# Performance work log

Measured on AMD Instinct MI355X. Metric: run time of the kernel, lower is better.

Reference implementation:

```python
import jax, jax.numpy as jnp
import numpy as np

N1 = 8000   # solute nodes
N2 = 8000   # solvent nodes
E = 128000  # edges per graph side (avg degree 16)
B = 128     # number of graphs in the batch
NFEAT, NHID, NCLS = 128, 256, 512
D = 2 * NCLS   # Set2Set input dim (1024)
H = D          # LSTM hidden = input_dim in DGL Set2Set


def setup_inputs() -> dict:
    key = jax.random.key(0)
    ks = jax.random.split(key, 24)
    w = lambda k, shp, fan: (jax.random.normal(k, shp, jnp.float32) / np.sqrt(fan))
    inp = {}
    inp["x1"] = jax.random.normal(ks[0], (N1, NFEAT), jnp.float32)
    inp["x2"] = jax.random.normal(ks[1], (N2, NFEAT), jnp.float32)
    inp["src1"] = jax.random.randint(ks[2], (E,), 0, N1, jnp.int32)
    inp["dst1"] = jax.random.randint(ks[3], (E,), 0, N1, jnp.int32)
    inp["src2"] = jax.random.randint(ks[4], (E,), 0, N2, jnp.int32)
    inp["dst2"] = jax.random.randint(ks[5], (E,), 0, N2, jnp.int32)
    inp["gid1"] = jnp.sort(jax.random.randint(ks[6], (N1,), 0, B, jnp.int32))
    inp["gid2"] = jnp.sort(jax.random.randint(ks[7], (N2,), 0, B, jnp.int32))
    # GraphConv weights (DGL stores W as [in, out]) + biases
    inp["W_gc1"] = w(ks[8], (NFEAT, NHID), NFEAT); inp["b_gc1"] = jnp.zeros((NHID,), jnp.float32)
    inp["W_gc2"] = w(ks[9], (NHID, NCLS), NHID);   inp["b_gc2"] = jnp.zeros((NCLS,), jnp.float32)
    inp["W_gc3"] = w(ks[10], (NFEAT, NHID), NFEAT); inp["b_gc3"] = jnp.zeros((NHID,), jnp.float32)
    inp["W_gc4"] = w(ks[11], (NHID, NCLS), NHID);   inp["b_gc4"] = jnp.zeros((NCLS,), jnp.float32)
    # Set2Set LSTM (input = 2*D, hidden = H), torch gate order i,f,g,o
    inp["W_ih"] = w(ks[12], (4 * H, 2 * D), 2 * D)
    inp["W_hh"] = w(ks[13], (4 * H, H), H)
    inp["b_ih"] = jnp.zeros((4 * H,), jnp.float32)
    inp["b_hh"] = jnp.zeros((4 * H,), jnp.float32)
    # MLP head
    inp["W_fc1"] = w(ks[14], (1024, 4096), 4096); inp["b_fc1"] = jnp.zeros((1024,), jnp.float32)
    inp["W_fc2"] = w(ks[15], (512, 1024), 1024);  inp["b_fc2"] = jnp.zeros((512,), jnp.float32)
    inp["W_fc3"] = w(ks[16], (1, 512), 512);      inp["b_fc3"] = jnp.zeros((1,), jnp.float32)
    return inp


def _gconv(x, src, dst, W, b, n):
    # DGL GraphConv, norm='both': D_out^{-1/2} scaling at src, sum over in-edges, D_in^{-1/2} at dst
    ones = jnp.ones(src.shape[0], x.dtype)
    outd = jnp.clip(jax.ops.segment_sum(ones, src, num_segments=n), 1.0)
    ind = jnp.clip(jax.ops.segment_sum(ones, dst, num_segments=n), 1.0)
    h = (x * (outd ** -0.5)[:, None]) @ W
    agg = jax.ops.segment_sum(h[src], dst, num_segments=n)   # sparse neighbor aggregation
    return agg * (ind ** -0.5)[:, None] + b


def _set2set(x, gid, Wih, Whh, bih, bhh):
    # DGL Set2Set, n_iters=2, 1-layer LSTM; x: [N, D], gid: [N] graph membership
    d = x.shape[1]
    q_star = jnp.zeros((B, 2 * d), x.dtype)
    h = jnp.zeros((B, d), x.dtype)
    c = jnp.zeros((B, d), x.dtype)
    for _ in range(2):
        gates = q_star @ Wih.T + h @ Whh.T + bih + bhh
        i, f, g, o = jnp.split(gates, 4, axis=1)
        c = jax.nn.sigmoid(f) * c + jax.nn.sigmoid(i) * jnp.tanh(g)
        h = jax.nn.sigmoid(o) * jnp.tanh(c)
        e = jnp.sum(x * h[gid], axis=1)                       # per-node attention logit
        m = jax.ops.segment_max(e, gid, num_segments=B)
        ex = jnp.exp(e - m[gid])
        s = jax.ops.segment_sum(ex, gid, num_segments=B)
        alpha = ex / s[gid]                                   # segment softmax
        r = jax.ops.segment_sum(alpha[:, None] * x, gid, num_segments=B)
        q_star = jnp.concatenate([h, r], axis=1)
    return q_star


def reference(x1, x2, src1, dst1, src2, dst2, gid1, gid2,
              W_gc1, b_gc1, W_gc2, b_gc2, W_gc3, b_gc3, W_gc4, b_gc4,
              W_ih, W_hh, b_ih, b_hh,
              W_fc1, b_fc1, W_fc2, b_fc2, W_fc3, b_fc3):
    s = jax.nn.relu(_gconv(x1, src1, dst1, W_gc1, b_gc1, N1))
    s = _gconv(s, src1, dst1, W_gc2, b_gc2, N1)
    v = jax.nn.relu(_gconv(x2, src2, dst2, W_gc3, b_gc3, N2))
    v = _gconv(v, src2, dst2, W_gc4, b_gc4, N2)
    # len_map = len1.T @ len2 == same-graph indicator for binary membership matrices
    len_map = (gid1[:, None] == gid2[None, :]).astype(s.dtype)
    imap = jnp.tanh(s @ v.T) * len_map                        # [N1, N2]
    solvent_prime = imap.T @ s                                # [N2, NCLS]
    solute_prime = imap @ v                                   # [N1, NCLS]
    sf = jnp.concatenate([s, solute_prime], axis=1)           # [N1, 2*NCLS]
    vf = jnp.concatenate([v, solvent_prime], axis=1)
    ss = _set2set(sf, gid1, W_ih, W_hh, b_ih, b_hh)           # [B, 4*NCLS]
    vs = _set2set(vf, gid2, W_ih, W_hh, b_ih, b_hh)
    z = jnp.concatenate([ss, vs], axis=1)                     # [B, 4096]
    z = jax.nn.relu(z @ W_fc1.T + b_fc1)
    z = jax.nn.relu(z @ W_fc2.T + b_fc2)
    return z @ W_fc3.T + b_fc3                                # [B, 1]
```

## Files before the change

### kernel.cpp

```cpp
#include <hip/hip_runtime.h>

#define DEV __device__ __forceinline__

typedef _Float16 half8 __attribute__((ext_vector_type(8)));
typedef _Float16 half4_t __attribute__((ext_vector_type(4)));
typedef float f32x4 __attribute__((ext_vector_type(4)));

DEV float ftanh(float x){
  float ax = fabsf(x);
  float e = __expf(-2.f*ax);
  float t = (1.f - e)/(1.f + e);
  return x < 0.f ? -t : t;
}
DEV float fsigm(float x){ return 1.f/(1.f + expf(-x)); }
DEV float wredsum(float v){
  #pragma unroll
  for (int o=32;o;o>>=1) v += __shfl_xor(v,o,64);
  return v;
}
DEV f32x4 MF(half8 a, half8 b, f32x4 c){
  return __builtin_amdgcn_mfma_f32_16x16x32_f16(a,b,c,0,0,0);
}
DEV void split8(float4 a0, float4 a1, half8& h, half8& l){
  float f[8] = {a0.x,a0.y,a0.z,a0.w,a1.x,a1.y,a1.z,a1.w};
  #pragma unroll
  for (int e=0;e<8;++e){
    _Float16 hh = (_Float16)f[e];
    h[e] = hh;
    l[e] = (_Float16)(f[e] - (float)hh);
  }
}

__global__ void k_zero_i32(int* __restrict__ p, int n){
  int i = blockIdx.x*256 + threadIdx.x; if (i<n) p[i]=0;
}

__global__ void k_hist2(const int* __restrict__ s1, const int* __restrict__ d1, int E1,
                        int* __restrict__ co1, int* __restrict__ ci1,
                        const int* __restrict__ s2, const int* __restrict__ d2, int E2,
                        int* __restrict__ co2, int* __restrict__ ci2){
  int e = blockIdx.x*256 + threadIdx.x;
  if (e < E1){ atomicAdd(&co1[s1[e]],1); atomicAdd(&ci1[d1[e]],1); }
  int f = e - E1;
  if (f >= 0 && f < E2){ atomicAdd(&co2[s2[f]],1); atomicAdd(&ci2[d2[f]],1); }
}

__global__ void k_scan2(const int* __restrict__ c1, int n1, int* __restrict__ r1,
                        const int* __restrict__ c2, int n2, int* __restrict__ r2){
  __shared__ int sm[1024];
  const int* cnt = blockIdx.x ? c2 : c1;
  int*       row = blockIdx.x ? r2 : r1;
  int n          = blockIdx.x ? n2 : n1;
  int t = threadIdx.x;
  int per = n/1024 + 1;
  int st = t*per;
  int s = 0;
  for (int i=st;i<st+per;++i) if (i<n) s += cnt[i];
  sm[t]=s; __syncthreads();
  for (int o=1;o<1024;o<<=1){
    int v = (t>=o)? sm[t-o]:0;
    __syncthreads();
    sm[t] += v;
    __syncthreads();
  }
  int base = sm[t]-s;
  for (int i=st;i<st+per;++i){
    if (i<=n) row[i]=base;
    if (i<n) base += cnt[i];
  }
}

__global__ void k_scale2(const int* __restrict__ co1, const int* __restrict__ ci1, int n1,
                         float* __restrict__ os1, float* __restrict__ is1,
                         const int* __restrict__ co2, const int* __restrict__ ci2, int n2,
                         float* __restrict__ os2, float* __restrict__ is2){
  int i = blockIdx.x*256+threadIdx.x;
  if (i<n1){
    int a = co1[i] > 1 ? co1[i] : 1;
    int b = ci1[i] > 1 ? ci1[i] : 1;
    os1[i] = 1.f/sqrtf((float)a);
    is1[i] = 1.f/sqrtf((float)b);
  }
  int j = i - n1;
  if (j>=0 && j<n2){
    int a = co2[j] > 1 ? co2[j] : 1;
    int b = ci2[j] > 1 ? ci2[j] : 1;
    os2[j] = 1.f/sqrtf((float)a);
    is2[j] = 1.f/sqrtf((float)b);
  }
}

__global__ void k_scatter2(const int* __restrict__ s1, const int* __restrict__ d1, int E1,
                           const int* __restrict__ row1, int* __restrict__ cur1, int* __restrict__ csr1,
                           const int* __restrict__ s2, const int* __restrict__ d2, int E2,
                           const int* __restrict__ row2, int* __restrict__ cur2, int* __restrict__ csr2){
  int e = blockIdx.x*256+threadIdx.x;
  if (e<E1){ int d=d1[e]; int p=atomicAdd(&cur1[d],1); csr1[row1[d]+p]=s1[e]; }
  int f = e - E1;
  if (f>=0 && f<E2){ int d=d2[f]; int p=atomicAdd(&cur2[d],1); csr2[row2[d]+p]=s2[f]; }
}

__global__ void k_goff2(const int* __restrict__ g1, int n1, int* __restrict__ o1,
                        const int* __restrict__ g2, int n2, int* __restrict__ o2, int B,
                        int* __restrict__ pb1, int* __restrict__ gm1,
                        int* __restrict__ pb2, int* __restrict__ gm2){
  __shared__ int sc[2][256];
  int t = threadIdx.x;
  const int* gid = (t>=256)? g2 : g1;
  int*      goff = (t>=256)? o2 : o1;
  int n          = (t>=256)? n2 : n1;
  const int side = t>>8, q = t & 255;
  if (q<=B){
    int lo=0, hi=n;
    while (lo<hi){ int mid=(lo+hi)>>1; if (gid[mid]<q) lo=mid+1; else hi=mid; }
    goff[q]=lo;
  }
  __syncthreads();
  int pc = 0;
  if (q < B){
    const int* go = side ? o2 : o1;
    int c = go[q+1]-go[q]; if (c>128) c=128;
    pc = (c+31)&~31;
  }
  sc[side][q] = pc;
  __syncthreads();
  for (int o=1;o<B;o<<=1){
    int v = (q>=o && q<B) ? sc[side][q-o] : 0;
    __syncthreads();
    if (q<B) sc[side][q] += v;
    __syncthreads();
  }
  if (q < B){
    int incl = sc[side][q];
    int pbv  = incl - pc;
    int* pb = side ? pb2 : pb1;
    int* gm = side ? gm2 : gm1;
    pb[q] = pbv;
    if (q == B-1) pb[B] = incl;
    int nb = pc>>5, b0 = pbv>>5;
    for (int k=0;k<nb;++k) gm[b0+k] = q;
  }
}

__global__ void k_agg_h(const float* __restrict__ x, int ldx, const float* __restrict__ osc,
                        const int* __restrict__ row, const int* __restrict__ csr,
                        _Float16* __restrict__ oh, _Float16* __restrict__ ol, int n, int f4shift){
  int F4 = 1<<f4shift;
  int node = blockIdx.x*(256>>f4shift) + (threadIdx.x>>f4shift);
  if (node>=n) return;
  int fc = threadIdx.x & (F4-1);
  int F = F4<<2;
  int rs=row[node], re=row[node+1];
  float ax=0, ay=0, az=0, aw=0;
  if (osc){
    for (int e=rs;e<re;++e){
      int s = csr[e];
      float sc = osc[s];
      const float4 v = *(const float4*)(x + (size_t)s*ldx + (fc<<2));
      ax += sc*v.x; ay += sc*v.y; az += sc*v.z; aw += sc*v.w;
    }
  } else {
    int e = rs;
    for (; e+1<re; e+=2){
      int s0 = csr[e], s1 = csr[e+1];
      const float4 v0 = *(const float4*)(x + (size_t)s0*ldx + (fc<<2));
      const float4 v1 = *(const float4*)(x + (size_t)s1*ldx + (fc<<2));
      ax += v0.x+v1.x; ay += v0.y+v1.y; az += v0.z+v1.z; aw += v0.w+v1.w;
    }
    if (e<re){
      int s0 = csr[e];
      const float4 v0 = *(const float4*)(x + (size_t)s0*ldx + (fc<<2));
      ax += v0.x; ay += v0.y; az += v0.z; aw += v0.w;
    }
  }
  half4_t hv, lv;
  hv.x = (_Float16)ax; lv.x = (_Float16)(ax - (float)hv.x);
  hv.y = (_Float16)ay; lv.y = (_Float16)(ay - (float)hv.y);
  hv.z = (_Float16)az; lv.z = (_Float16)(az - (float)hv.z);
  hv.w = (_Float16)aw; lv.w = (_Float16)(aw - (float)hv.w);
  size_t o = (size_t)node*F + (fc<<2);
  *(half4_t*)(oh + o) = hv;
  *(half4_t*)(ol + o) = lv;
}

__global__ void k_wpack4(const float* __restrict__ W0, const float* __restrict__ W1,
                         const float* __restrict__ W2, const float* __restrict__ W3,
                         _Float16* __restrict__ h0, _Float16* __restrict__ l0,
                         _Float16* __restrict__ h1, _Float16* __restrict__ l1,
                         _Float16* __restrict__ h2, _Float16* __restrict__ l2,
                         _Float16* __restrict__ h3, _Float16* __restrict__ l3){
  int w = blockIdx.y;
  const float* W = (w==0)?W0:(w==1)?W1:(w==2)?W2:W3;
  _Float16* oh = (w==0)?h0:(w==1)?h1:(w==2)?h2:h3;
  _Float16* ol = (w==0)?l0:(w==1)?l1:(w==2)?l2:l3;
  int K   = (w&1)? 256 : 128;
  int nsh = (w&1)? 9 : 8;
  int i = blockIdx.x*256 + threadIdx.x;
  if (i >= (K<<nsh)) return;
  int k = i >> nsh, n = i & ((1<<nsh)-1);
  float v = W[i];
  _Float16 h = (_Float16)v;
  _Float16 l = (_Float16)(v - (float)h);
  size_t p = (((size_t)(k>>3)<<nsh) + n)*8 + (k&7);
  oh[p] = h; ol[p] = l;
}

__global__ __launch_bounds__(256)
void k_gconv_mfma(const _Float16* __restrict__ Ah0, const _Float16* __restrict__ Al0,
                  const _Float16* __restrict__ Ah1, const _Float16* __restrict__ Al1,
                  const _Float16* __restrict__ Bh0, const _Float16* __restrict__ Bl0,
                  const _Float16* __restrict__ Bh1, const _Float16* __restrict__ Bl1,
                  float* __restrict__ C0, float* __restrict__ C1, int ldc,
                  int M0, int M1, int N, int K,
                  const float* __restrict__ rs0, const float* __restrict__ rs1,
                  const float* __restrict__ bi0, const float* __restrict__ bi1, int relu,
                  const float* __restrict__ po0, const float* __restrict__ po1)
{
  __shared__ __align__(16) _Float16 As[2][4096];
  __shared__ __align__(16) _Float16 Bs[2][4096];

  const int gx = gridDim.x, gxy = gridDim.x*gridDim.y;
  const int nwg = gxy*2;
  int fid = blockIdx.x + gx*blockIdx.y + gxy*blockIdx.z;
  int q = nwg>>3, r = nwg&7;
  int xcd = fid & 7, idx = fid >> 3;
  int sid = (xcd<r ? xcd*(q+1) : r*(q+1)+(xcd-r)*q) + idx;
  const int z  = sid / gxy;  int rem = sid - z*gxy;
  const int by = rem / gx,  bx = rem - by*gx;

  const _Float16* Ah = z ? Ah1 : Ah0;
  const _Float16* Al = z ? Al1 : Al0;
  const _Float16* Bh = z ? Bh1 : Bh0;
  const _Float16* Bl = z ? Bl1 : Bl0;
  float*       C  = z ? C1 : C0;
  const float* rsc = z ? rs1 : rs0;
  const float* bia = z ? bi1 : bi0;
  const float* po  = z ? po1 : po0;
  const int M = z ? M1 : M0;

  const int row0 = by << 7;
  const int col0 = bx << 7;
  if (row0 >= ((M+127)&~127)) return;

  const int tid = threadIdx.x;
  const int am  = tid >> 2;
  const int akb = tid & 3;
  const int bn  = tid & 127;
  const int bkb = tid >> 7;
  const int wid = tid >> 6, lane = tid & 63;
  const int wr = wid >> 1, wc = wid & 1;
  const int lr = lane & 15, lg = lane >> 4;

  const size_t ldb8 = (size_t)N * 8;
  f32x4 acc[4][4] = {};

  const int kpt = K >> 5;
  const int nt  = 3 * kpt;

  half8 ga0, ga1, gb0, gb1;
  {
    const _Float16* Ap = Ah + (size_t)(row0 + am) * K + (akb<<3);
    ga0 = *(const half8*)(Ap);
    ga1 = *(const half8*)(Ap + (size_t)64 * K);
    const _Float16* Bp = Bh + (size_t)bkb * ldb8 + (size_t)(col0 + bn) * 8;
    gb0 = *(const half8*)(Bp);
    gb1 = *(const half8*)(Bp + 2*ldb8);
  }
  *(half8*)&As[0][(akb*128 + am)*8]        = ga0;
  *(half8*)&As[0][(akb*128 + am + 64)*8]   = ga1;
  *(half8*)&Bs[0][(bkb*128 + bn)*8]        = gb0;
  *(half8*)&Bs[0][((bkb+2)*128 + bn)*8]    = gb1;
  __syncthreads();

  int term = 0, kk = 32;
  if (kk == K){ kk = 0; term = 1; }
  for (int t = 0; t < nt; ++t){
    const int cb = t & 1;
    if (t + 1 < nt){
      const _Float16* Asrc = (term == 1) ? Al : Ah;
      const _Float16* Bsrc = (term == 2) ? Bl : Bh;
      const _Float16* Ap = Asrc + (size_t)(row0 + am) * K + kk + (akb<<3);
      ga0 = *(const half8*)(Ap);
      ga1 = *(const half8*)(Ap + (size_t)64 * K);
      const _Float16* Bp = Bsrc + (size_t)((kk>>3) + bkb) * ldb8 + (size_t)(col0 + bn) * 8;
      gb0 = *(const half8*)(Bp);
      gb1 = *(const half8*)(Bp + 2*ldb8);
      kk += 32; if (kk == K){ kk = 0; ++term; }
    }
    {
      const _Float16* Abase = &As[cb][((lg<<7) + (wr<<6) + lr)<<3];
      const _Float16* Bbase = &Bs[cb][((lg<<7) + (wc<<6) + lr)<<3];
      half8 af[4], bf[4];
      #pragma unroll
      for (int i=0;i<4;++i){
        af[i] = *(const half8*)(Abase + i*128);
        bf[i] = *(const half8*)(Bbase + i*128);
      }
      #pragma unroll
      for (int mi=0; mi<4; ++mi){
        #pragma unroll
        for (int ni=0; ni<4; ++ni){
          acc[mi][ni] = __builtin_amdgcn_mfma_f32_16x16x32_f16(af[mi], bf[ni], acc[mi][ni], 0, 0, 0);
        }
      }
    }
    if (t + 1 < nt){
      const int nb_ = cb ^ 1;
      *(half8*)&As[nb_][(akb*128 + am)*8]      = ga0;
      *(half8*)&As[nb_][(akb*128 + am + 64)*8] = ga1;
      *(half8*)&Bs[nb_][(bkb*128 + bn)*8]      = gb0;
      *(half8*)&Bs[nb_][((bkb+2)*128 + bn)*8]  = gb1;
    }
    __syncthreads();
  }

  #pragma unroll
  for (int ni = 0; ni < 4; ++ni){
    int cc = col0 + (wc<<6) + (ni<<4) + lr;
    float bv = bia ? bia[cc] : 0.f;
    #pragma unroll
    for (int mi = 0; mi < 4; ++mi){
      int rbase = row0 + (wr<<6) + (mi<<4) + (lg<<2);
      #pragma unroll
      for (int j = 0; j < 4; ++j){
        int rr = rbase + j;
        if (rr < M){
          float rs_ = rsc ? rsc[rr] : 1.f;
          float v = acc[mi][ni][j]*rs_ + bv;
          if (relu) v = fmaxf(v, 0.f);
          if (po) v *= po[rr];
          C[(size_t)rr*ldc + cc] = v;
        }
      }
    }
  }
}

__global__ __launch_bounds__(256)
void k_pack(const float* __restrict__ sf, const float* __restrict__ vf,
            const int* __restrict__ go1, const int* __restrict__ go2,
            const int* __restrict__ pb1, const int* __restrict__ pb2,
            const int* __restrict__ gm1, const int* __restrict__ gm2,
            _Float16* __restrict__ p1h, _Float16* __restrict__ p1l,
            _Float16* __restrict__ p2h, _Float16* __restrict__ p2l, int B)
{
  __shared__ float st[32][516];
  const int side = blockIdx.y;
  const float* x = side ? vf : sf;
  const int* go = side ? go2 : go1;
  const int* pb = side ? pb2 : pb1;
  const int* gm = side ? gm2 : gm1;
  _Float16* ph = side ? p2h : p1h;
  _Float16* pl = side ? p2l : p1l;
  const int u = blockIdx.x;
  if (u*32 >= pb[B]) return;
  const int g = gm[u];
  const int j0 = u*32 - pb[g];
  const int base = go[g];
  int cnt = go[g+1]-base; if (cnt>128) cnt=128;
  const int t = threadIdx.x;
  const int r = t>>3, f0 = (t&7)<<2;
  const bool valid = (j0 + r) < cnt;
  const float* src = x + (size_t)(base + j0 + r)*1024;
  #pragma unroll
  for (int q=0;q<16;++q){
    int f = f0 + (q<<5);
    float4 vv;
    if (valid) vv = *(const float4*)(src + f);
    else { vv.x=0.f; vv.y=0.f; vv.z=0.f; vv.w=0.f; }
    *(float4*)&st[r][f] = vv;
  }
  __syncthreads();
  #pragma unroll
  for (int q=0;q<8;++q){
    int u2 = t + (q<<8);
    int jg = u2>>9, f = u2&511;
    half8 h8, l8;
    #pragma unroll
    for (int e=0;e<8;++e){
      float vvv = st[(jg<<3)+e][f];
      _Float16 hh = (_Float16)vvv;
      h8[e]=hh; l8[e]=(_Float16)(vvv-(float)hh);
    }
    size_t a = ((size_t)((u<<2)+jg)<<12) + ((size_t)f<<3);
    *(half8*)(ph + a) = h8;
    *(half8*)(pl + a) = l8;
  }
}

__global__ __launch_bounds__(256)
void k_T(const float* __restrict__ sf, const float* __restrict__ vf,
         const int* __restrict__ go1, const int* __restrict__ go2,
         _Float16* __restrict__ Th, _Float16* __restrict__ Tl, int B)
{
  __shared__ __align__(16) _Float16 Ahs[64*136 + 8];
  __shared__ __align__(16) _Float16 Als[64*136 + 8];
  __shared__ __align__(16) _Float16 Bhs[2][2048];
  __shared__ __align__(16) _Float16 Bls[2][2048];
  const int g = blockIdx.x, rt = blockIdx.y;
  int gR = go1[g]; int c1 = go1[g+1]-gR; if (c1>128) c1=128;
  int gO = go2[g]; int c2 = go2[g+1]-gO; if (c2>128) c2=128;
  const int c1_32 = (c1+31)&~31, c2_32 = (c2+31)&~31;
  if ((rt<<4) >= c1_32 || c2_32 == 0) return;
  const int tid = threadIdx.x;
  {
    const int r = tid >> 4;
    const int f0 = (tid & 15) << 5;
    const int row = (rt<<4) + r;
    const bool val = row < c1;
    const float* src = sf + (size_t)(gR + row)*1024 + f0;
    #pragma unroll
    for (int q=0;q<4;++q){
      float4 v0, v1;
      if (val){
        v0 = *(const float4*)(src + (q<<3));
        v1 = *(const float4*)(src + (q<<3) + 4);
      } else {
        v0.x=0.f; v0.y=0.f; v0.z=0.f; v0.w=0.f; v1 = v0;
      }
      half8 h,l; split8(v0,v1,h,l);
      const int a = ((f0>>3) + q)*136 + (r<<3);
      *(half8*)&Ahs[a] = h; *(half8*)&Als[a] = l;
    }
  }
  const int w = tid>>6, lane = tid&63, lr = lane&15, lg = lane>>4;
  const int bc = tid>>2, bfg = tid&3, bf = bfg<<3;
  const int bwr = (bfg<<9) + ((bc ^ (bfg<<2))<<3);
  const int ncc = (c2_32 + 63) >> 6;
  _Float16* T0h = Th + ((size_t)g<<14);
  _Float16* T0l = Tl + ((size_t)g<<14);
  _Float16* T1h = Th + ((size_t)(B + g)<<14);
  _Float16* T1l = Tl + ((size_t)(B + g)<<14);
  for (int cc=0; cc<ncc; ++cc){
    const int cbase = cc<<6;
    const int colr = cbase + bc;
    const bool bval = colr < c2;
    const float* bsrc = vf + (size_t)(gO + colr)*1024 + bf;
    {
      float4 v0, v1;
      if (bval){ v0 = *(const float4*)(bsrc); v1 = *(const float4*)(bsrc + 4); }
      else { v0.x=0.f; v0.y=0.f; v0.z=0.f; v0.w=0.f; v1 = v0; }
      half8 h,l; split8(v0,v1,h,l);
      *(half8*)&Bhs[0][bwr] = h; *(half8*)&Bls[0][bwr] = l;
    }
    __syncthreads();
    f32x4 acc = {0.f,0.f,0.f,0.f};
    const int col_l = (w<<4) + lr;
    const int ba = (lg<<9) + ((col_l ^ (lg<<2))<<3);
    for (int kc=0; kc<16; ++kc){
      float4 p0, p1;
      if (kc+1<16){
        if (bval){
          const float* s = bsrc + ((kc+1)<<5);
          p0 = *(const float4*)s; p1 = *(const float4*)(s + 4);
        } else { p0.x=0.f; p0.y=0.f; p0.z=0.f; p0.w=0.f; p1 = p0; }
      }
      const int aa = ((kc<<2)+lg)*136 + (lr<<3);
      half8 ah = *(const half8*)&Ahs[aa];
      half8 al = *(const half8*)&Als[aa];
      half8 bh = *(const half8*)&Bhs[kc&1][ba];
      half8 bl = *(const half8*)&Bls[kc&1][ba];
      acc = MF(ah,bh,acc);
      acc = MF(al,bh,acc);
      acc = MF(ah,bl,acc);
      if (kc+1<16){
        half8 h,l; split8(p0,p1,h,l);
        *(half8*)&Bhs[(kc+1)&1][bwr] = h; *(half8*)&Bls[(kc+1)&1][bwr] = l;
      }
      __syncthreads();
    }
    const int col = cbase + col_l;
    if (col < c2_32){
      half4_t t1h, t1l;
      #pragma unroll
      for (int qq=0;qq<4;++qq){
        int r = (rt<<4) + (lg<<2) + qq;
        float t = (r < c1 && col < c2) ? ftanh(acc[qq]) : 0.f;
        _Float16 hh = (_Float16)t;
        _Float16 ll = (_Float16)(t - (float)hh);
        T0h[(r<<7) + col] = hh;
        T0l[(r<<7) + col] = ll;
        t1h[qq] = hh; t1l[qq] = ll;
      }
      const int r0 = (rt<<4) + (lg<<2);
      *(half4_t*)&T1h[(col<<7) + r0] = t1h;
      *(half4_t*)&T1l[(col<<7) + r0] = t1l;
    }
  }
}

__global__ __launch_bounds__(256)
void k_apply(const _Float16* __restrict__ Th, const _Float16* __restrict__ Tl,
             const _Float16* __restrict__ p1h, const _Float16* __restrict__ p1l,
             const _Float16* __restrict__ p2h, const _Float16* __restrict__ p2l,
             const int* __restrict__ go1, const int* __restrict__ go2,
             const int* __restrict__ pb1, const int* __restrict__ pb2,
             float* __restrict__ sf, float* __restrict__ vf, int B)
{
  const int side = blockIdx.x, g = blockIdx.y, ft = blockIdx.z;
  const int* goR = side ? go2 : go1;
  const int* goO = side ? go1 : go2;
  const int* pbO = side ? pb1 : pb2;
  const _Float16* oph = side ? p1h : p2h;
  const _Float16* opl = side ? p1l : p2l;
  float* outp = side ? vf : sf;
  int gR = goR[g]; int cR = goR[g+1]-gR; if (cR>128) cR=128;
  int gO = goO[g]; int cO = goO[g+1]-gO; if (cO>128) cO=128;
  if (cR <= 0) return;
  const int pO = pbO[g];
  const int cO32 = (cO+31)&~31;
  const int MR = ((cR+15)&~15)>>4;
  const _Float16* Tph = Th + ((size_t)(side*B + g)<<14);
  const _Float16* Tpl = Tl + ((size_t)(side*B + g)<<14);
  const int tid = threadIdx.x, w = tid>>6, lane = tid&63;
  const int lr = lane&15, lg = lane>>4;
  const int f0 = (ft<<8) + (w<<6);
  for (int rc = 0; rc < MR; rc += 4){
    f32x4 acc[4][4];
    #pragma unroll
    for (int a_=0;a_<4;++a_)
      #pragma unroll
      for (int b_=0;b_<4;++b_) acc[a_][b_] = (f32x4){0.f,0.f,0.f,0.f};
    for (int k0=0; k0<cO32; k0+=32){
      half8 bh[4], bl[4];
      #pragma unroll
      for (int nj=0;nj<4;++nj){
        size_t a = ((size_t)((pO + k0)>>3) + lg)*4096 + (size_t)(f0 + (nj<<4) + lr)*8;
        bh[nj] = *(const half8*)(oph + a);
        bl[nj] = *(const half8*)(opl + a);
      }
      #pragma unroll
      for (int mi=0;mi<4;++mi){
        if (rc + mi < MR){
          int a = ((((rc+mi)<<4) + lr)<<7) + k0 + (lg<<3);
          half8 th_ = *(const half8*)&Tph[a];
          half8 tl_ = *(const half8*)&Tpl[a];
          #pragma unroll
          for (int nj=0;nj<4;++nj){
            acc[mi][nj] = MF(th_, bh[nj], acc[mi][nj]);
            acc[mi][nj] = MF(tl_, bh[nj], acc[mi][nj]);
            acc[mi][nj] = MF(th_, bl[nj], acc[mi][nj]);
          }
        }
      }
    }
    #pragma unroll
    for (int mi=0;mi<4;++mi){
      if (rc + mi < MR){
        #pragma unroll
        for (int nj=0;nj<4;++nj){
          #pragma unroll
          for (int qq=0;qq<4;++qq){
            int r = (((rc+mi)<<4)) + (lg<<2) + qq;
            if (r < cR)
              outp[(size_t)(gR + r)*1024 + 512 + f0 + (nj<<4) + lr] = acc[mi][nj][qq];
          }
        }
      }
    }
  }
}

__global__ __launch_bounds__(256)
void k_gemmsk(const float* __restrict__ Ab, size_t AsideOff, int lda,
              const float* __restrict__ Bm, int ldb,
              float* __restrict__ P, int M, int N, int kchunk)
{
  __shared__ float As[2][16][132];
  __shared__ float Bs[2][16][68];
  const int tid = threadIdx.x;
  const int col0 = (int)blockIdx.x << 6;
  const int kbeg = (int)blockIdx.z * kchunk;
  const float* A = Ab + (size_t)blockIdx.y * AsideOff;
  const int ar = tid >> 1, ak = (tid & 1) << 3;
  const int br = tid >> 2, bk = (tid & 3) << 2;
  const int tx = tid & 15, ty = tid >> 4;
  const float* Arow = A + (size_t)ar * lda + kbeg + ak;
  const float* Brow = Bm + (size_t)(col0 + br) * ldb + kbeg + bk;
  float acc[8][4] = {};
  float4 a0 = *(const float4*)(Arow);
  float4 a1 = *(const float4*)(Arow + 4);
  float4 b0 = *(const float4*)(Brow);
  As[0][ak+0][ar]=a0.x; As[0][ak+1][ar]=a0.y; As[0][ak+2][ar]=a0.z; As[0][ak+3][ar]=a0.w;
  As[0][ak+4][ar]=a1.x; As[0][ak+5][ar]=a1.y; As[0][ak+6][ar]=a1.z; As[0][ak+7][ar]=a1.w;
  Bs[0][bk+0][br]=b0.x; Bs[0][bk+1][br]=b0.y; Bs[0][bk+2][br]=b0.z; Bs[0][bk+3][br]=b0.w;
  __syncthreads();
  const int nt = kchunk >> 4;
  for (int t = 0; t < nt; ++t){
    const int cb = t & 1;
    if (t + 1 < nt){
      int k0 = (t + 1) << 4;
      a0 = *(const float4*)(Arow + k0);
      a1 = *(const float4*)(Arow + k0 + 4);
      b0 = *(const float4*)(Brow + k0);
    }
    #pragma unroll
    for (int kk = 0; kk < 16; ++kk){
      float4 b4 = *(const float4*)&Bs[cb][kk][tx << 2];
      float4 a4 = *(const float4*)&As[cb][kk][ty << 3];
      float4 a5 = *(const float4*)&As[cb][kk][(ty << 3) + 4];
      acc[0][0]+=a4.x*b4.x; acc[0][1]+=a4.x*b4.y; acc[0][2]+=a4.x*b4.z; acc[0][3]+=a4.x*b4.w;
      acc[1][0]+=a4.y*b4.x; acc[1][1]+=a4.y*b4.y; acc[1][2]+=a4.y*b4.z; acc[1][3]+=a4.y*b4.w;
      acc[2][0]+=a4.z*b4.x; acc[2][1]+=a4.z*b4.y; acc[2][2]+=a4.z*b4.z; acc[2][3]+=a4.z*b4.w;
      acc[3][0]+=a4.w*b4.x; acc[3][1]+=a4.w*b4.y; acc[3][2]+=a4.w*b4.z; acc[3][3]+=a4.w*b4.w;
      acc[4][0]+=a5.x*b4.x; acc[4][1]+=a5.x*b4.y; acc[4][2]+=a5.x*b4.z; acc[4][3]+=a5.x*b4.w;
      acc[5][0]+=a5.y*b4.x; acc[5][1]+=a5.y*b4.y; acc[5][2]+=a5.y*b4.z; acc[5][3]+=a5.y*b4.w;
      acc[6][0]+=a5.z*b4.x; acc[6][1]+=a5.z*b4.y; acc[6][2]+=a5.z*b4.z; acc[6][3]+=a5.z*b4.w;
      acc[7][0]+=a5.w*b4.x; acc[7][1]+=a5.w*b4.y; acc[7][2]+=a5.w*b4.z; acc[7][3]+=a5.w*b4.w;
    }
    if (t + 1 < nt){
      const int nb = cb ^ 1;
      As[nb][ak+0][ar]=a0.x; As[nb][ak+1][ar]=a0.y; As[nb][ak+2][ar]=a0.z; As[nb][ak+3][ar]=a0.w;
      As[nb][ak+4][ar]=a1.x; As[nb][ak+5][ar]=a1.y; As[nb][ak+6][ar]=a1.z; As[nb][ak+7][ar]=a1.w;
      Bs[nb][bk+0][br]=b0.x; Bs[nb][bk+1][br]=b0.y; Bs[nb][bk+2][br]=b0.z; Bs[nb][bk+3][br]=b0.w;
    }
    __syncthreads();
  }
  float* Pz = P + (size_t)(blockIdx.y*gridDim.z + blockIdx.z) * M * N;
  #pragma unroll
  for (int i = 0; i < 8; ++i){
    int rr = (ty << 3) + i;
    float4 v = {acc[i][0], acc[i][1], acc[i][2], acc[i][3]};
    *(float4*)(Pz + (size_t)rr*N + col0 + (tx<<2)) = v;
  }
}

__global__ void k_red_bias(const float* __restrict__ P, int split, int MN, int N,
                           const float* __restrict__ bias, float* __restrict__ C, int relu){
  int i = blockIdx.x*256 + threadIdx.x;
  if (i >= MN) return;
  float v = bias[i & (N-1)];
  for (int s=0;s<split;++s) v += P[(size_t)s*MN + i];
  if (relu) v = fmaxf(v, 0.f);
  C[i] = v;
}

__global__ void k_lstm1(const float* __restrict__ bih, const float* __restrict__ bhh,
                        float* __restrict__ c1, float* __restrict__ h1){
  int j = blockIdx.x*256 + threadIdx.x;
  if (j >= 1024) return;
  float gi = bih[j]        + bhh[j];
  float gg = bih[j+2048]   + bhh[j+2048];
  float go = bih[j+3072]   + bhh[j+3072];
  float cc = fsigm(gi)*ftanh(gg);
  c1[j] = cc;
  h1[j] = fsigm(go)*ftanh(cc);
}

__global__ void k_gemv_u(const float* __restrict__ Wih, const float* __restrict__ Whh,
                         const float* __restrict__ bih, const float* __restrict__ bhh,
                         const float* __restrict__ h1, float* __restrict__ u){
  int w = (blockIdx.x*256 + threadIdx.x)>>6;
  int lane = threadIdx.x & 63;
  if (w >= 4096) return;
  const float* wi = Wih + (size_t)w*2048;
  const float* wh = Whh + (size_t)w*1024;
  float acc = 0.f;
  #pragma unroll
  for (int qq=0;qq<4;++qq){
    int o = qq*256 + (lane<<2);
    float4 hv = *(const float4*)(h1 + o);
    float4 a  = *(const float4*)(wi + o);
    float4 b  = *(const float4*)(wh + o);
    acc += hv.x*(a.x+b.x) + hv.y*(a.y+b.y) + hv.z*(a.z+b.z) + hv.w*(a.w+b.w);
  }
  acc = wredsum(acc);
  if (lane==0) u[w] = acc + bih[w] + bhh[w];
}

__global__ __launch_bounds__(256)
void k_attn(const float* __restrict__ sf, const float* __restrict__ vf,
            const int* __restrict__ go1, const int* __restrict__ go2,
            const float* __restrict__ hbase, size_t hSideOff, int hstride,
            float* __restrict__ outbase, size_t oSideOff, int ldout)
{
  __shared__ float hs[1024];
  __shared__ float ech[1024];
  __shared__ float red[8];
  int side = blockIdx.y;
  const float* x = side? vf : sf;
  const int* goff = side? go2 : go1;
  const float* hsrc = hbase + (size_t)side*hSideOff;
  float* outp = outbase + (size_t)side*oSideOff;
  int b = blockIdx.x, t = threadIdx.x;
  int i0 = goff[b], i1 = goff[b+1];
  int lane = t & 63, wv = t >> 6;
  { float4 hv = *(const float4*)(hsrc + (size_t)b*hstride + (t<<2));
    *(float4*)&hs[t<<2] = hv; }
  __syncthreads();
  float m = -3.0e38f, s = 0.f;
  float ax=0, ay=0, az=0, aw=0;
  for (int c = i0; c < i1; c += 1024){
    int ce = c + 1024; if (ce > i1) ce = i1;
    int n = ce - c;
    float wmax = -3.0e38f;
    for (int i = c + wv; i < ce; i += 4){
      const float* xr = x + (size_t)i*1024;
      float d = 0.f;
      #pragma unroll
      for (int qq=0;qq<4;++qq){
        int o = qq*256 + (lane<<2);
        float4 xv = *(const float4*)(xr+o);
        float4 h4 = *(const float4*)&hs[o];
        d += xv.x*h4.x + xv.y*h4.y + xv.z*h4.z + xv.w*h4.w;
      }
      d = wredsum(d);
      if (lane==0) ech[i-c] = d;
      wmax = fmaxf(wmax, d);
    }
    if (lane==0) red[wv] = wmax;
    __syncthreads();
    float cm = fmaxf(fmaxf(red[0],red[1]), fmaxf(red[2],red[3]));
    float nm = fmaxf(m, cm);
    float scale = __expf(m - nm);
    s *= scale; ax*=scale; ay*=scale; az*=scale; aw*=scale;
    float ps = 0.f;
    for (int k = t; k < n; k += 256) ps += __expf(ech[k]-nm);
    ps = wredsum(ps);
    __syncthreads();
    if (lane==0) red[wv] = ps;
    __syncthreads();
    s += red[0]+red[1]+red[2]+red[3];
    for (int k = 0; k < n; ++k){
      float w = __expf(ech[k]-nm);
      float4 xv = *(const float4*)(x + (size_t)(c+k)*1024 + (t<<2));
      ax += w*xv.x; ay += w*xv.y; az += w*xv.z; aw += w*xv.w;
    }
    m = nm;
    __syncthreads();
  }
  float inv = (i1>i0 && s>0.f) ? 1.f/s : 0.f;
  float4 o = {ax*inv, ay*inv, az*inv, aw*inv};
  *(float4*)(outp + (size_t)b*ldout + (t<<2)) = o;
}

__global__ void k_lstm2_red(const float* __restrict__ Pb, size_t PsideOff, int split,
                            const float* __restrict__ u, const float* __restrict__ c1,
                            float* __restrict__ z, int B){
  int idx = blockIdx.x*256 + threadIdx.x;
  if (idx >= B*1024) return;
  int side = blockIdx.y;
  const float* P = Pb + (size_t)side*PsideOff;
  int b = idx >> 10, j = idx & 1023;
  float gi=u[j], gf=u[j+1024], gg=u[j+2048], go=u[j+3072];
  const float* g = P + (size_t)b*4096;
  for (int s=0;s<split;++s){
    const float* gs = g + (size_t)s*B*4096;
    gi += gs[j]; gf += gs[j+1024]; gg += gs[j+2048]; go += gs[j+3072];
  }
  float cc = fsigm(gf)*c1[j] + fsigm(gi)*ftanh(gg);
  z[(size_t)b*4096 + side*2048 + j] = fsigm(go)*ftanh(cc);
}

__global__ void k_fc3(const float* __restrict__ z2, const float* __restrict__ w3,
                      const float* __restrict__ b3, float* __restrict__ out, int B){
  int wv = (blockIdx.x*256+threadIdx.x)>>6;
  int lane = threadIdx.x & 63;
  if (wv >= B) return;
  const float* zr = z2 + (size_t)wv*512;
  float acc=0.f;
  #pragma unroll
  for (int qq=0;qq<2;++qq){
    int o = qq*256 + (lane<<2);
    float4 a  = *(const float4*)(zr + o);
    float4 ww = *(const float4*)(w3 + o);
    acc += a.x*ww.x + a.y*ww.y + a.z*ww.z + a.w*ww.w;
  }
  acc = wredsum(acc);
  if (lane==0) out[wv] = acc + b3[0];
}

extern "C" void kernel_launch(void* const* d_in, const int* in_sizes, int n_in,
                              void* d_out, int out_size, void* d_ws, size_t ws_size,
                              hipStream_t stream)
{
  const float* x1  = (const float*)d_in[0];
  const float* x2  = (const float*)d_in[1];
  const int* src1  = (const int*)d_in[2];
  const int* dst1  = (const int*)d_in[3];
  const int* src2  = (const int*)d_in[4];
  const int* dst2  = (const int*)d_in[5];
  const int* gid1  = (const int*)d_in[6];
  const int* gid2  = (const int*)d_in[7];
  const float* Wg1 = (const float*)d_in[8];  const float* bg1 = (const float*)d_in[9];
  const float* Wg2 = (const float*)d_in[10]; const float* bg2 = (const float*)d_in[11];
  const float* Wg3 = (const float*)d_in[12]; const float* bg3 = (const float*)d_in[13];
  const float* Wg4 = (const float*)d_in[14]; const float* bg4 = (const float*)d_in[15];
  const float* Wih = (const float*)d_in[16]; const float* Whh = (const float*)d_in[17];
  const float* bih = (const float*)d_in[18]; const float* bhh = (const float*)d_in[19];
  const float* Wf1 = (const float*)d_in[20]; const float* bf1 = (const float*)d_in[21];
  const float* Wf2 = (const float*)d_in[22]; const float* bf2 = (const float*)d_in[23];
  const float* Wf3 = (const float*)d_in[24]; const float* bf3 = (const float*)d_in[25];
  float* out = (float*)d_out;

  const int N1 = in_sizes[0]/128;
  const int N2 = in_sizes[1]/128;
  const int E1 = in_sizes[2];
  const int E2 = in_sizes[4];
  const int B  = out_size;
  const int NM = N1>N2?N1:N2;

  char* base = (char*)d_ws; size_t off=0;
  auto alloc = [&](size_t bytes)->void*{ void* p = base+off; off += (bytes+255)&~(size_t)255; return p; };

  int* zr   = (int*)alloc(sizeof(int)*(size_t)(3*N1+3*N2));
  int* co1=zr, *ci1=zr+N1, *cur1=zr+2*N1;
  int* co2=zr+3*N1, *ci2=zr+3*N1+N2, *cur2=zr+3*N1+2*N2;
  int* row1 = (int*)alloc(sizeof(int)*(size_t)(N1+1));
  int* row2 = (int*)alloc(sizeof(int)*(size_t)(N2+1));
  int* csr1 = (int*)alloc(sizeof(int)*(size_t)E1);
  int* csr2 = (int*)alloc(sizeof(int)*(size_t)E2);
  int* go1  = (int*)alloc(sizeof(int)*(size_t)(B+1));
  int* go2  = (int*)alloc(sizeof(int)*(size_t)(B+1));
  int* pb1  = (int*)alloc(sizeof(int)*(size_t)(B+1));
  int* pb2  = (int*)alloc(sizeof(int)*(size_t)(B+1));
  int* gm1  = (int*)alloc(sizeof(int)*1024);
  int* gm2  = (int*)alloc(sizeof(int)*1024);
  float* os1 = (float*)alloc(sizeof(float)*(size_t)N1);
  float* is1 = (float*)alloc(sizeof(float)*(size_t)N1);
  float* os2 = (float*)alloc(sizeof(float)*(size_t)N2);
  float* is2 = (float*)alloc(sizeof(float)*(size_t)N2);
  _Float16* a1h = (_Float16*)alloc(sizeof(_Float16)*(size_t)(NM+128)*256);
  _Float16* a1l = (_Float16*)alloc(sizeof(_Float16)*(size_t)(NM+128)*256);
  _Float16* a2h = (_Float16*)alloc(sizeof(_Float16)*(size_t)(NM+128)*256);
  _Float16* a2l = (_Float16*)alloc(sizeof(_Float16)*(size_t)(NM+128)*256);
  _Float16* wg1h = (_Float16*)alloc(sizeof(_Float16)*32768);
  _Float16* wg1l = (_Float16*)alloc(sizeof(_Float16)*32768);
  _Float16* wg2h = (_Float16*)alloc(sizeof(_Float16)*131072);
  _Float16* wg2l = (_Float16*)alloc(sizeof(_Float16)*131072);
  _Float16* wg3h = (_Float16*)alloc(sizeof(_Float16)*32768);
  _Float16* wg3l = (_Float16*)alloc(sizeof(_Float16)*32768);
  _Float16* wg4h = (_Float16*)alloc(sizeof(_Float16)*131072);
  _Float16* wg4l = (_Float16*)alloc(sizeof(_Float16)*131072);
  float* sf  = (float*)alloc(sizeof(float)*(size_t)(N1+128)*1024);
  float* vf  = (float*)alloc(sizeof(float)*(size_t)(N2+128)*1024);
  float* h1 = (float*)alloc(sizeof(float)*1024);
  float* c1 = (float*)alloc(sizeof(float)*1024);
  float* u  = (float*)alloc(sizeof(float)*4096);
  float* r1 = (float*)alloc(sizeof(float)*(size_t)2*B*1024);
  float* z1 = (float*)alloc(sizeof(float)*(size_t)B*1024);
  float* z2 = (float*)alloc(sizeof(float)*(size_t)B*512);
  float* z  = (float*)alloc(sizeof(float)*(size_t)B*4096);
  _Float16* Tqh = (_Float16*)alloc(sizeof(_Float16)*(size_t)2*B*16384);
  _Float16* Tql = (_Float16*)alloc(sizeof(_Float16)*(size_t)2*B*16384);
  const int PN = ((NM + 32*B + 63)&~63) + 64;
  const size_t PE = (size_t)PN*512;
  size_t packedBytes = 4*PE*sizeof(_Float16);
  size_t pbufBytes   = sizeof(float)*(size_t)16*B*1024*4;
  char* uni = (char*)alloc(packedBytes > pbufBytes ? packedBytes : pbufBytes);
  _Float16* p1h = (_Float16*)uni;
  _Float16* p1l = p1h + PE;
  _Float16* p2h = p1l + PE;
  _Float16* p2l = p2h + PE;
  float* Pbuf = (float*)uni;
  if (off > ws_size) return;

  float* hb1 = sf + 512;
  float* hb2 = vf + 512;

  dim3 blk(256);

  k_wpack4<<<dim3(512,4),blk,0,stream>>>(Wg1,Wg2,Wg3,Wg4,
                                         wg1h,wg1l, wg2h,wg2l, wg3h,wg3l, wg4h,wg4l);

  k_zero_i32<<<(3*N1+3*N2+255)/256, blk, 0, stream>>>(zr, 3*N1+3*N2);
  k_hist2<<<(E1+E2+255)/256, blk, 0, stream>>>(src1,dst1,E1,co1,ci1, src2,dst2,E2,co2,ci2);
  k_scan2<<<2,1024,0,stream>>>(ci1,N1,row1, ci2,N2,row2);
  k_scale2<<<(N1+N2+255)/256,blk,0,stream>>>(co1,ci1,N1,os1,is1, co2,ci2,N2,os2,is2);
  k_scatter2<<<(E1+E2+255)/256,blk,0,stream>>>(src1,dst1,E1,row1,cur1,csr1, src2,dst2,E2,row2,cur2,csr2);
  k_goff2<<<1,512,0,stream>>>(gid1,N1,go1, gid2,N2,go2, B, pb1,gm1, pb2,gm2);

  int gy = (NM+127)/128;
  k_agg_h<<<(N1+7)/8,blk,0,stream>>>(x1,128, os1,row1,csr1, a1h,a1l, N1,5);
  k_agg_h<<<(N2+7)/8,blk,0,stream>>>(x2,128, os2,row2,csr2, a2h,a2l, N2,5);
  k_gconv_mfma<<<dim3(2,gy,2),blk,0,stream>>>(a1h,a1l, a2h,a2l,
                                              wg1h,wg1l, wg3h,wg3l,
                                              hb1,hb2,1024, N1,N2, 256,128,
                                              is1,is2, bg1,bg3, 1, os1,os2);
  k_agg_h<<<(N1+3)/4,blk,0,stream>>>(hb1,1024, nullptr,row1,csr1, a1h,a1l, N1,6);
  k_agg_h<<<(N2+3)/4,blk,0,stream>>>(hb2,1024, nullptr,row2,csr2, a2h,a2l, N2,6);
  k_gconv_mfma<<<dim3(4,gy,2),blk,0,stream>>>(a1h,a1l, a2h,a2l,
                                              wg2h,wg2l, wg4h,wg4l,
                                              sf,vf,1024, N1,N2, 512,256,
                                              is1,is2, bg2,bg4, 0, nullptr,nullptr);

  const int GMAX = NM/32 + B + 2;
  k_pack<<<dim3(GMAX,2),blk,0,stream>>>(sf,vf, go1,go2, pb1,pb2, gm1,gm2,
                                        p1h,p1l, p2h,p2l, B);
  k_T<<<dim3(B,8),blk,0,stream>>>(sf,vf, go1,go2, Tqh,Tql, B);
  k_apply<<<dim3(2,B,2),blk,0,stream>>>(Tqh,Tql, p1h,p1l, p2h,p2l,
                                        go1,go2, pb1,pb2, sf,vf, B);

  k_lstm1<<<4,blk,0,stream>>>(bih,bhh,c1,h1);
  k_gemv_u<<<1024,blk,0,stream>>>(Wih,Whh,bih,bhh,h1,u);

  k_attn<<<dim3(B,2),blk,0,stream>>>(sf,vf,go1,go2, h1,0,0, r1,(size_t)B*1024,1024);
  k_gemmsk<<<dim3(64,2,4),blk,0,stream>>>(r1,(size_t)B*1024,1024, Wih+1024,2048, Pbuf, 128,4096,256);
  k_lstm2_red<<<dim3((B*1024+255)/256,2),blk,0,stream>>>(Pbuf,(size_t)4*B*4096,4, u,c1, z,B);
  k_attn<<<dim3(B,2),blk,0,stream>>>(sf,vf,go1,go2, z,2048,4096, z+1024,2048,4096);

  k_gemmsk<<<dim3(16,1,16),blk,0,stream>>>(z,0,4096, Wf1,4096, Pbuf, 128,1024,256);
  k_red_bias<<<(B*1024+255)/256,blk,0,stream>>>(Pbuf,16,B*1024,1024,bf1,z1,1);
  k_gemmsk<<<dim3(8,1,8),blk,0,stream>>>(z1,0,1024, Wf2,1024, Pbuf, 128,512,128);
  k_red_bias<<<(B*512+255)/256,blk,0,stream>>>(Pbuf,8,B*512,512,bf2,z2,1);
  k_fc3<<<(B*64+255)/256,blk,0,stream>>>(z2,Wf3,bf3,out,B);
}
```

Measured before the change: 385.6 us.

## Use split-fp16 MFMA GEMM for Set2Set input and FC1 projections

Adds a kernel that transposes W_ih's attention half and W_fc1 into an fp16 hi/lo split layout, plus a split-K MFMA GEMM that converts activations to hi/lo fp16 on the fly and uses three MFMAs per tile to approximate fp32 accuracy. These replace the scalar fp32 split-K GEMMs for the LSTM input projection and FC1. FC1 now uses 32 K-splits instead of 16, which means a larger partial buffer and more reduction work. Weight packing runs on every call, adding about 16M elements of conversion traffic.

```diff
diff --git a/kernel.cpp b/kernel.cpp
--- a/kernel.cpp
+++ b/kernel.cpp
@@ -203,6 +203,38 @@
   _Float16 l = (_Float16)(v - (float)h);
   size_t p = (((size_t)(k>>3)<<nsh) + n)*8 + (k&7);
   oh[p] = h; ol[p] = l;
+}
+
+__global__ __launch_bounds__(256)
+void k_wpackT(const float* __restrict__ W, int ldw, int N,
+              _Float16* __restrict__ Bh, _Float16* __restrict__ Bl){
+  __shared__ float st[32][260];
+  const int k0 = (int)blockIdx.x << 8;
+  const int n0 = (int)blockIdx.y << 5;
+  const int t = threadIdx.x;
+  const int r = t >> 3, la = t & 7;
+  const float* src = W + (size_t)(n0 + r)*ldw + k0;
+  #pragma unroll
+  for (int q=0;q<8;++q){
+    int f = (la<<2) + (q<<5);
+    *(float4*)&st[r][f] = *(const float4*)(src + f);
+  }
+  __syncthreads();
+  const int nl = t & 31;
+  #pragma unroll
+  for (int j=0;j<4;++j){
+    int kbl = (t>>5) + (j<<3);
+    half8 h8, l8;
+    #pragma unroll
+    for (int e=0;e<8;++e){
+      float v = st[nl][(kbl<<3)+e];
+      _Float16 hh = (_Float16)v;
+      h8[e]=hh; l8[e]=(_Float16)(v-(float)hh);
+    }
+    size_t a = ((size_t)((k0>>3)+kbl)*N + n0 + nl)*8;
+    *(half8*)(Bh + a) = h8;
+    *(half8*)(Bl + a) = l8;
+  }
 }
 
 __global__ __launch_bounds__(256)
@@ -625,6 +657,88 @@
   }
 }
 
+__global__ __launch_bounds__(256)
+void k_gemmsk_h(const float* __restrict__ Ab, size_t AsideOff, int lda,
+                const _Float16* __restrict__ Bhp, const _Float16* __restrict__ Blp,
+                float* __restrict__ P, int N, int kchunk)
+{
+  __shared__ __align__(16) _Float16 Ahs[2][4096];
+  __shared__ __align__(16) _Float16 Als[2][4096];
+  const int tid = threadIdx.x;
+  const int col0 = (int)blockIdx.x << 7;
+  const int kbeg = (int)blockIdx.z * kchunk;
+  const float* A = Ab + (size_t)blockIdx.y * AsideOff;
+  const int ar = tid >> 1, aq = (tid & 1) << 4;
+  const int wid = tid>>6, lane = tid&63;
+  const int wr = wid>>1, wc = wid&1;
+  const int lr = lane&15, lg = lane>>4;
+  const float* Arow = A + (size_t)ar*lda + kbeg + aq;
+  const int akb = aq>>3;
+  f32x4 acc[4][4] = {};
+  const int nc = kchunk >> 5;
+  float4 g0,g1,g2,g3;
+  g0 = *(const float4*)(Arow);     g1 = *(const float4*)(Arow+4);
+  g2 = *(const float4*)(Arow+8);   g3 = *(const float4*)(Arow+12);
+  {
+    half8 h,l;
+    split8(g0,g1,h,l);
+    *(half8*)&Ahs[0][(akb*128+ar)*8] = h;     *(half8*)&Als[0][(akb*128+ar)*8] = l;
+    split8(g2,g3,h,l);
+    *(half8*)&Ahs[0][((akb+1)*128+ar)*8] = h; *(half8*)&Als[0][((akb+1)*128+ar)*8] = l;
+  }
+  __syncthreads();
+  for (int c=0;c<nc;++c){
+    const int cb = c&1;
+    if (c+1<nc){
+      const float* p = Arow + ((c+1)<<5);
+      g0 = *(const float4*)(p);    g1 = *(const float4*)(p+4);
+      g2 = *(const float4*)(p+8);  g3 = *(const float4*)(p+12);
+    }
+    const size_t kb0 = (size_t)((kbeg + (c<<5)) >> 3) + lg;
+    half8 bh[4], bl[4];
+    #pragma unroll
+    for (int ni=0;ni<4;++ni){
+      size_t a = (kb0*N + col0 + (wc<<6) + (ni<<4) + lr)*8;
+      bh[ni] = *(const half8*)(Bhp + a);
+      bl[ni] = *(const half8*)(Blp + a);
+    }
+    #pragma unroll
+    for (int mi=0;mi<4;++mi){
+      int aa = ((lg<<7) + (wr<<6) + (mi<<4) + lr)<<3;
+      half8 ah = *(const half8*)&Ahs[cb][aa];
+      half8 al = *(const half8*)&Als[cb][aa];
+      #pragma unroll
+      for (int ni=0;ni<4;++ni){
+        acc[mi][ni] = MF(ah,bh[ni],acc[mi][ni]);
+        acc[mi][ni] = MF(al,bh[ni],acc[mi][ni]);
+        acc[mi][ni] = MF(ah,bl[ni],acc[mi][ni]);
+      }
+    }
+    if (c+1<nc){
+      const int nb = cb^1;
+      half8 h,l;
+      split8(g0,g1,h,l);
+      *(half8*)&Ahs[nb][(akb*128+ar)*8] = h;     *(half8*)&Als[nb][(akb*128+ar)*8] = l;
+      split8(g2,g3,h,l);
+      *(half8*)&Ahs[nb][((akb+1)*128+ar)*8] = h; *(half8*)&Als[nb][((akb+1)*128+ar)*8] = l;
+    }
+    __syncthreads();
+  }
+  float* Pz = P + (size_t)(blockIdx.y*gridDim.z + blockIdx.z)*128*N;
+  #pragma unroll
+  for (int mi=0;mi<4;++mi){
+    #pragma unroll
+    for (int ni=0;ni<4;++ni){
+      int cc2 = col0 + (wc<<6) + (ni<<4) + lr;
+      #pragma unroll
+      for (int j=0;j<4;++j){
+        int rr2 = (wr<<6) + (mi<<4) + (lg<<2) + j;
+        Pz[(size_t)rr2*N + cc2] = acc[mi][ni][j];
+      }
+    }
+  }
+}
+
 __global__ void k_red_bias(const float* __restrict__ P, int split, int MN, int N,
                            const float* __restrict__ bias, float* __restrict__ C, int relu){
   int i = blockIdx.x*256 + threadIdx.x;
@@ -832,6 +946,10 @@
   _Float16* wg3l = (_Float16*)alloc(sizeof(_Float16)*32768);
   _Float16* wg4h = (_Float16*)alloc(sizeof(_Float16)*131072);
   _Float16* wg4l = (_Float16*)alloc(sizeof(_Float16)*131072);
+  _Float16* wihh = (_Float16*)alloc(sizeof(_Float16)*(size_t)4096*1024);
+  _Float16* wihl = (_Float16*)alloc(sizeof(_Float16)*(size_t)4096*1024);
+  _Float16* wf1h = (_Float16*)alloc(sizeof(_Float16)*(size_t)1024*4096);
+  _Float16* wf1l = (_Float16*)alloc(sizeof(_Float16)*(size_t)1024*4096);
   float* sf  = (float*)alloc(sizeof(float)*(size_t)(N1+128)*1024);
   float* vf  = (float*)alloc(sizeof(float)*(size_t)(N2+128)*1024);
   float* h1 = (float*)alloc(sizeof(float)*1024);
@@ -846,7 +964,7 @@
   const int PN = ((NM + 32*B + 63)&~63) + 64;
   const size_t PE = (size_t)PN*512;
   size_t packedBytes = 4*PE*sizeof(_Float16);
-  size_t pbufBytes   = sizeof(float)*(size_t)16*B*1024*4;
+  size_t pbufBytes   = sizeof(float)*(size_t)32*B*1024*4;
   char* uni = (char*)alloc(packedBytes > pbufBytes ? packedBytes : pbufBytes);
   _Float16* p1h = (_Float16*)uni;
   _Float16* p1l = p1h + PE;
@@ -862,6 +980,8 @@
 
   k_wpack4<<<dim3(512,4),blk,0,stream>>>(Wg1,Wg2,Wg3,Wg4,
                                          wg1h,wg1l, wg2h,wg2l, wg3h,wg3l, wg4h,wg4l);
+  k_wpackT<<<dim3(4,128),blk,0,stream>>>(Wih+1024, 2048, 4096, wihh, wihl);
+  k_wpackT<<<dim3(16,32),blk,0,stream>>>(Wf1, 4096, 1024, wf1h, wf1l);
 
   k_zero_i32<<<(3*N1+3*N2+255)/256, blk, 0, stream>>>(zr, 3*N1+3*N2);
   k_hist2<<<(E1+E2+255)/256, blk, 0, stream>>>(src1,dst1,E1,co1,ci1, src2,dst2,E2,co2,ci2);
@@ -895,12 +1015,12 @@
   k_gemv_u<<<1024,blk,0,stream>>>(Wih,Whh,bih,bhh,h1,u);
 
   k_attn<<<dim3(B,2),blk,0,stream>>>(sf,vf,go1,go2, h1,0,0, r1,(size_t)B*1024,1024);
-  k_gemmsk<<<dim3(64,2,4),blk,0,stream>>>(r1,(size_t)B*1024,1024, Wih+1024,2048, Pbuf, 128,4096,256);
+  k_gemmsk_h<<<dim3(32,2,4),blk,0,stream>>>(r1,(size_t)B*1024,1024, wihh,wihl, Pbuf, 4096,256);
   k_lstm2_red<<<dim3((B*1024+255)/256,2),blk,0,stream>>>(Pbuf,(size_t)4*B*4096,4, u,c1, z,B);
   k_attn<<<dim3(B,2),blk,0,stream>>>(sf,vf,go1,go2, z,2048,4096, z+1024,2048,4096);
 
-  k_gemmsk<<<dim3(16,1,16),blk,0,stream>>>(z,0,4096, Wf1,4096, Pbuf, 128,1024,256);
-  k_red_bias<<<(B*1024+255)/256,blk,0,stream>>>(Pbuf,16,B*1024,1024,bf1,z1,1);
+  k_gemmsk_h<<<dim3(8,1,32),blk,0,stream>>>(z,0,4096, wf1h,wf1l, Pbuf, 1024,128);
+  k_red_bias<<<(B*1024+255)/256,blk,0,stream>>>(Pbuf,32,B*1024,1024,bf1,z1,1);
   k_gemmsk<<<dim3(8,1,8),blk,0,stream>>>(z1,0,1024, Wf2,1024, Pbuf, 128,512,128);
   k_red_bias<<<(B*512+255)/256,blk,0,stream>>>(Pbuf,8,B*512,512,bf2,z2,1);
   k_fc3<<<(B*64+255)/256,blk,0,stream>>>(z2,Wf3,bf3,out,B);
```

After: 384.5 us. Within noise of the previous version (-0.3%).
